# Kernel tuning notes

Measured on AMD Instinct MI355X. Metric: run time of the kernel, lower is better.

## Reference

```python
import jax, jax.numpy as jnp
import numpy as np

H, W = 1024, 1024        # heatmap resolution
C = 128                  # n_targets (clusters)
N_ITER = 8               # n_iterations


def setup_inputs() -> dict:
    key = jax.random.key(0)
    k1, k2 = jax.random.split(key)
    # clusters live in pixel coordinate space [0,H) x [0,W)
    clusters = jax.random.uniform(k1, (C, 2), dtype=jnp.float32) * jnp.array([H, W], dtype=jnp.float32)
    heatmap = jax.random.uniform(k2, (H, W), dtype=jnp.float32)
    return {"clusters": clusters, "heatmap": heatmap}


def reference(clusters, heatmap):
    # pixel coordinate grid [H, W, 2] with (row, col) ordering, matching
    # clusters[c,0]-row, clusters[c,1]-col in the original code
    rows = jnp.arange(H, dtype=jnp.float32)
    cols = jnp.arange(W, dtype=jnp.float32)
    coords = jnp.stack(jnp.meshgrid(rows, cols, indexing='ij'), axis=-1)  # [H, W, 2]

    def step(cs, _):
        # Euclidean distance from every pixel to every cluster, clamped to >= 1
        diff = coords[:, :, None, :] - cs[None, None, :, :]          # [H, W, C, 2]
        dist = jnp.maximum(1.0, jnp.sqrt(jnp.sum(diff * diff, axis=-1)))  # [H, W, C]
        assign = jnp.argmin(dist, axis=-1)                            # [H, W] nearest cluster
        best_dist = jnp.min(dist, axis=-1)                            # [H, W]
        # weighted scatter-add of pixel coords into their nearest cluster
        contrib = coords * (heatmap / best_dist)[..., None]           # [H, W, 2]
        new_cs = jax.ops.segment_sum(contrib.reshape(-1, 2), assign.reshape(-1), num_segments=C)
        return new_cs.astype(jnp.float32), None

    cs, _ = jax.lax.scan(step, clusters, None, length=N_ITER)
    return cs
```

## Files before the change

kernel.cpp:

```cpp
#include <hip/hip_runtime.h>
#include <float.h>

constexpr int H = 1024, W = 1024, C = 128, N_ITER = 8;
constexpr int TPB = 256;
constexpr int TILE = 32;
constexpr int PPT = 4;
constexpr int K = 32;
constexpr int SLOTS = 2 * C;

__global__ __launch_bounds__(TPB) void kmeans_step(
    const float* __restrict__ cur0,
    const float* __restrict__ prevShards,
    const float* __restrict__ heatmap,
    float* __restrict__ outShards)
{
    __shared__ float2 cls[C];
    __shared__ float2 cand[C];
    __shared__ int    candIdx[C];
    __shared__ float  waveMin[2];
    __shared__ int    waveCnt[2];
    __shared__ float  acc[SLOTS];
    __shared__ unsigned char dupf[C];

    const int tid   = threadIdx.x;
    const int tileR = (blockIdx.x >> 5) * TILE;
    const int tileC = (blockIdx.x & 31) * TILE;

    acc[tid] = 0.0f;
    if (tid < C) dupf[tid] = 0;

    float coord;
    if (prevShards) {
        float s = 0.0f;
#pragma unroll
        for (int k = 0; k < K; ++k) s += prevShards[k * SLOTS + tid];
        coord = s;
    } else {
        coord = cur0[tid];
    }
    ((float*)cls)[tid] = coord;
    __syncthreads();

    const int    di  = tid & (C - 1);
    const float2 dme = cls[di];

    float dcen = 0.0f;
    if (tid < C) {
        const float dxr = dme.x - ((float)tileR + 15.5f);
        const float dyc = dme.y - ((float)tileC + 15.5f);
        dcen = sqrtf(dxr * dxr + dyc * dyc);
        float m = dcen;
#pragma unroll
        for (int off = 32; off > 0; off >>= 1)
            m = fminf(m, __shfl_xor(m, off));
        if ((tid & 63) == 0) waveMin[tid >> 6] = m;
    }

    {
        const int kLo = (tid < C) ? 1 : 33;
#pragma unroll 8
        for (int kk = 0; kk < 32; ++kk) {
            const int k = kLo + kk;
            const int j = (di + k) & (C - 1);
            const float2 o = cls[j];
            if (o.x == dme.x && o.y == dme.y)
                dupf[(di + k < C) ? (di + k) : di] = 1;
        }
    }
    __syncthreads();

    bool keep = false;
    int  pre  = 0;
    if (tid < C) {
        const float thr = fminf(waveMin[0], waveMin[1]) + 44.84062f;
        keep = (dcen <= thr) && (dupf[tid] == 0);
        const unsigned long long mask = __ballot(keep);
        const int lane = tid & 63;
        pre = __popcll(mask & ((1ull << lane) - 1ull));
        if (lane == 0) waveCnt[tid >> 6] = __popcll(mask);
    }
    __syncthreads();
    if (keep) {
        const int pos = pre + ((tid >= 64) ? waveCnt[0] : 0);
        cand[pos]    = cls[tid];
        candIdx[pos] = tid;
    }
    __syncthreads();

    const int nCand = waveCnt[0] + waveCnt[1];

    const int   rowIn = tid >> 3;
    const float fr    = (float)(tileR + rowIn);
    const int   col0  = tileC + (tid & 7) * PPT;
    const float4 h4   = *(const float4*)(heatmap + (size_t)(tileR + rowIn) * W + col0);

    float hval[PPT] = { h4.x, h4.y, h4.z, h4.w };
    float colf[PPT], best[PPT];
    int   bi[PPT];
#pragma unroll
    for (int p = 0; p < PPT; ++p) {
        colf[p] = (float)(col0 + p);
        best[p] = FLT_MAX;
        bi[p]   = 0;
    }

    for (int k = 0; k < nCand; ++k) {
        const float2 cl = cand[k];
        const int    ci = candIdx[k];
        const float  dx  = fr - cl.x;
        const float  dx2 = dx * dx;
#pragma unroll
        for (int p = 0; p < PPT; ++p) {
            const float dy  = colf[p] - cl.y;
            const float d2  = fmaf(dy, dy, dx2);
            const float key = fmaxf(d2, 1.0f);
            const bool  lt  = key < best[p];
            bi[p]   = lt ? ci  : bi[p];
            best[p] = lt ? key : best[p];
        }
    }

#pragma unroll
    for (int p = 0; p < PPT; ++p) {
        const float bd  = fmaxf(1.0f, sqrtf(best[p]));
        const float wgt = hval[p] / bd;
        float v0 = fr      * wgt;
        float v1 = colf[p] * wgt;
        const int b0 = __shfl(bi[p], 0);
        if (__ballot(bi[p] == b0) == 0xFFFFFFFFFFFFFFFFull) {
#pragma unroll
            for (int off = 32; off > 0; off >>= 1) {
                v0 += __shfl_xor(v0, off);
                v1 += __shfl_xor(v1, off);
            }
            if ((tid & 63) == 0) {
                unsafeAtomicAdd(&acc[2 * b0 + 0], v0);
                unsafeAtomicAdd(&acc[2 * b0 + 1], v1);
            }
        } else {
            unsafeAtomicAdd(&acc[2 * bi[p] + 0], v0);
            unsafeAtomicAdd(&acc[2 * bi[p] + 1], v1);
        }
    }
    __syncthreads();

    const float a = acc[tid];
    if (a != 0.0f)
        unsafeAtomicAdd(&outShards[(blockIdx.x & (K - 1)) * SLOTS + tid], a);
}

__global__ __launch_bounds__(SLOTS) void kmeans_finalize(
    const float* __restrict__ shards,
    float* __restrict__ out)
{
    const int tid = threadIdx.x;
    float s = 0.0f;
#pragma unroll
    for (int k = 0; k < K; ++k) s += shards[k * SLOTS + tid];
    out[tid] = s;
}

extern "C" void kernel_launch(void* const* d_in, const int* in_sizes, int n_in,
                              void* d_out, int out_size, void* d_ws, size_t ws_size,
                              hipStream_t stream) {
    const float* clusters = (const float*)d_in[0];
    const float* heatmap  = (const float*)d_in[1];
    float* out = (float*)d_out;

    float* shards = (float*)d_ws;
    const size_t perIter = (size_t)K * SLOTS;

    hipMemsetAsync(shards, 0, N_ITER * perIter * sizeof(float), stream);

    for (int it = 0; it < N_ITER; ++it) {
        const float* prev = (it == 0) ? nullptr : (shards + (it - 1) * perIter);
        float* dst = shards + it * perIter;
        kmeans_step<<<H, TPB, 0, stream>>>(clusters, prev, heatmap, dst);
    }
    kmeans_finalize<<<1, SLOTS, 0, stream>>>(shards + (N_ITER - 1) * perIter, out);
}
```

Before: 143.3 us.

## Fuse all iterations into one persistent kernel with a coordinator block and flag barriers

Replaces the eight per-iteration launches and the finalize launch with one kernel. Block 0 acts as a coordinator: it waits on distributed arrival counters, reduces the shards, runs the duplicate-cluster check once, and publishes sign-encoded centroids to replicated buffers. Worker blocks spin on those buffers for the next iteration. This removes launch gaps, keeps the heatmap tile in registers across iterations, and moves the duplicate check off the workers. The cost is a 1025-block grid that depends on all blocks being co-resident (launch bounds raised to 4 blocks per CU), with a risk of deadlock or spin overhead if they are not.

```diff
diff --git a/kernel.cpp b/kernel.cpp
--- a/kernel.cpp
+++ b/kernel.cpp
@@ -7,12 +7,24 @@
 constexpr int PPT = 4;
 constexpr int K = 32;
 constexpr int SLOTS = 2 * C;
-
-__global__ __launch_bounds__(TPB) void kmeans_step(
+constexpr int NBLK = (H / TILE) * (W / TILE);
+constexpr int NCNT = 128;
+constexpr int CNT_STRIDE = 16;
+constexpr int ARRIVE_DEPTH = NBLK / NCNT;
+constexpr int NREP = 16;
+constexpr unsigned SIGNB = 0x80000000u;
+
+__device__ __forceinline__ void waitVmem() {
+    asm volatile("s_waitcnt vmcnt(0)" ::: "memory");
+}
+
+__global__ __launch_bounds__(TPB, 4) void kmeans_fused(
     const float* __restrict__ cur0,
-    const float* __restrict__ prevShards,
     const float* __restrict__ heatmap,
-    float* __restrict__ outShards)
+    float* __restrict__ shards,
+    int*   __restrict__ barCnt,
+    unsigned* __restrict__ clsPub,
+    float* __restrict__ out)
 {
     __shared__ float2 cls[C];
     __shared__ float2 cand[C];
@@ -22,142 +34,188 @@
     __shared__ float  acc[SLOTS];
     __shared__ unsigned char dupf[C];
 
-    const int tid   = threadIdx.x;
-    const int tileR = (blockIdx.x >> 5) * TILE;
-    const int tileC = (blockIdx.x & 31) * TILE;
-
-    acc[tid] = 0.0f;
-    if (tid < C) dupf[tid] = 0;
-
-    float coord;
-    if (prevShards) {
-        float s = 0.0f;
-#pragma unroll
-        for (int k = 0; k < K; ++k) s += prevShards[k * SLOTS + tid];
-        coord = s;
-    } else {
-        coord = cur0[tid];
+    const int tid = threadIdx.x;
+    const int bid = blockIdx.x;
+
+    if (bid == 0) {
+        for (int it = 0; it < N_ITER; ++it) {
+            if (tid < NCNT) {
+                int* cptr = barCnt + ((size_t)it * NCNT + tid) * CNT_STRIDE;
+                while (__hip_atomic_load(cptr, __ATOMIC_RELAXED,
+                                         __HIP_MEMORY_SCOPE_AGENT) < ARRIVE_DEPTH)
+                    __builtin_amdgcn_s_sleep(1);
+            }
+            __syncthreads();
+
+            const float* b = shards + (size_t)it * K * SLOTS + tid;
+            float v[K];
+#pragma unroll
+            for (int k = 0; k < K; ++k)
+                v[k] = __hip_atomic_load(b + (size_t)k * SLOTS,
+                                         __ATOMIC_RELAXED, __HIP_MEMORY_SCOPE_AGENT);
+            float s = 0.0f;
+#pragma unroll
+            for (int k = 0; k < K; ++k) s += v[k];
+
+            if (it == N_ITER - 1) {
+                out[tid] = s;
+                return;
+            }
+
+            if (tid < C) dupf[tid] = 0;
+            ((float*)cls)[tid] = s;
+            __syncthreads();
+            {
+                const int    sdi  = tid & (C - 1);
+                const float2 sdme = cls[sdi];
+                const int kLo = (tid < C) ? 1 : 33;
+#pragma unroll 8
+                for (int kk = 0; kk < 32; ++kk) {
+                    const int k = kLo + kk;
+                    const int j = (sdi + k) & (C - 1);
+                    const float2 o = cls[j];
+                    if (o.x == sdme.x && o.y == sdme.y)
+                        dupf[(sdi + k < C) ? (sdi + k) : sdi] = 1;
+                }
+            }
+            __syncthreads();
+
+            const float pv = dupf[tid >> 1] ? (float)INFINITY : s;
+            const unsigned enc = __float_as_uint(pv) ^ SIGNB;
+            unsigned* pb = clsPub + (size_t)it * NREP * SLOTS;
+#pragma unroll
+            for (int r = 0; r < NREP; ++r)
+                __hip_atomic_store(pb + r * SLOTS + tid, enc,
+                                   __ATOMIC_RELAXED, __HIP_MEMORY_SCOPE_AGENT);
+        }
+        return;
     }
-    ((float*)cls)[tid] = coord;
-    __syncthreads();
-
-    const int    di  = tid & (C - 1);
-    const float2 dme = cls[di];
-
-    float dcen = 0.0f;
-    if (tid < C) {
-        const float dxr = dme.x - ((float)tileR + 15.5f);
-        const float dyc = dme.y - ((float)tileC + 15.5f);
-        dcen = sqrtf(dxr * dxr + dyc * dyc);
-        float m = dcen;
-#pragma unroll
-        for (int off = 32; off > 0; off >>= 1)
-            m = fminf(m, __shfl_xor(m, off));
-        if ((tid & 63) == 0) waveMin[tid >> 6] = m;
-    }
-
-    {
-        const int kLo = (tid < C) ? 1 : 33;
-#pragma unroll 8
-        for (int kk = 0; kk < 32; ++kk) {
-            const int k = kLo + kk;
-            const int j = (di + k) & (C - 1);
-            const float2 o = cls[j];
-            if (o.x == dme.x && o.y == dme.y)
-                dupf[(di + k < C) ? (di + k) : di] = 1;
-        }
-    }
-    __syncthreads();
-
-    bool keep = false;
-    int  pre  = 0;
-    if (tid < C) {
-        const float thr = fminf(waveMin[0], waveMin[1]) + 44.84062f;
-        keep = (dcen <= thr) && (dupf[tid] == 0);
-        const unsigned long long mask = __ballot(keep);
-        const int lane = tid & 63;
-        pre = __popcll(mask & ((1ull << lane) - 1ull));
-        if (lane == 0) waveCnt[tid >> 6] = __popcll(mask);
-    }
-    __syncthreads();
-    if (keep) {
-        const int pos = pre + ((tid >= 64) ? waveCnt[0] : 0);
-        cand[pos]    = cls[tid];
-        candIdx[pos] = tid;
-    }
-    __syncthreads();
-
-    const int nCand = waveCnt[0] + waveCnt[1];
+
+    const int wid   = bid - 1;
+    const int tileR = (wid >> 5) * TILE;
+    const int tileC = (wid & 31) * TILE;
 
     const int   rowIn = tid >> 3;
     const float fr    = (float)(tileR + rowIn);
     const int   col0  = tileC + (tid & 7) * PPT;
     const float4 h4   = *(const float4*)(heatmap + (size_t)(tileR + rowIn) * W + col0);
-
     float hval[PPT] = { h4.x, h4.y, h4.z, h4.w };
-    float colf[PPT], best[PPT];
-    int   bi[PPT];
-#pragma unroll
-    for (int p = 0; p < PPT; ++p) {
-        colf[p] = (float)(col0 + p);
-        best[p] = FLT_MAX;
-        bi[p]   = 0;
+    float colf[PPT];
+#pragma unroll
+    for (int p = 0; p < PPT; ++p) colf[p] = (float)(col0 + p);
+
+    for (int it = 0; it < N_ITER; ++it) {
+        float coord;
+        if (it == 0) {
+            coord = cur0[tid];
+        } else {
+            const unsigned* src = clsPub
+                + ((size_t)(it - 1) * NREP + (wid & (NREP - 1))) * SLOTS;
+            unsigned u;
+            for (;;) {
+                u = __hip_atomic_load(src + tid, __ATOMIC_RELAXED,
+                                      __HIP_MEMORY_SCOPE_AGENT);
+                if (__ballot(u != 0u) == 0xFFFFFFFFFFFFFFFFull) break;
+                __builtin_amdgcn_s_sleep(4);
+            }
+            coord = __uint_as_float(u ^ SIGNB);
+        }
+
+        acc[tid] = 0.0f;
+        ((float*)cls)[tid] = coord;
+        __syncthreads();
+
+        float dcen = 0.0f;
+        if (tid < C) {
+            const float2 cl = cls[tid];
+            const float dxr = cl.x - ((float)tileR + 15.5f);
+            const float dyc = cl.y - ((float)tileC + 15.5f);
+            dcen = sqrtf(dxr * dxr + dyc * dyc);
+            float m = dcen;
+#pragma unroll
+            for (int off = 32; off > 0; off >>= 1)
+                m = fminf(m, __shfl_xor(m, off));
+            if ((tid & 63) == 0) waveMin[tid >> 6] = m;
+        }
+        __syncthreads();
+
+        bool keep = false;
+        int  pre  = 0;
+        if (tid < C) {
+            const float thr = fminf(waveMin[0], waveMin[1]) + 44.84062f;
+            keep = (dcen <= thr);
+            const unsigned long long mask = __ballot(keep);
+            const int lane = tid & 63;
+            pre = __popcll(mask & ((1ull << lane) - 1ull));
+            if (lane == 0) waveCnt[tid >> 6] = __popcll(mask);
+        }
+        __syncthreads();
+        if (keep) {
+            const int pos = pre + ((tid >= 64) ? waveCnt[0] : 0);
+            cand[pos]    = cls[tid];
+            candIdx[pos] = tid;
+        }
+        __syncthreads();
+
+        const int nCand = waveCnt[0] + waveCnt[1];
+
+        float best[PPT];
+        int   bi[PPT];
+#pragma unroll
+        for (int p = 0; p < PPT; ++p) { best[p] = FLT_MAX; bi[p] = 0; }
+
+        for (int k = 0; k < nCand; ++k) {
+            const float2 cl = cand[k];
+            const int    ci = candIdx[k];
+            const float  dx  = fr - cl.x;
+            const float  dx2 = dx * dx;
+#pragma unroll
+            for (int p = 0; p < PPT; ++p) {
+                const float dy  = colf[p] - cl.y;
+                const float d2  = fmaf(dy, dy, dx2);
+                const float key = fmaxf(d2, 1.0f);
+                const bool  lt  = key < best[p];
+                bi[p]   = lt ? ci  : bi[p];
+                best[p] = lt ? key : best[p];
+            }
+        }
+
+#pragma unroll
+        for (int p = 0; p < PPT; ++p) {
+            const float bd  = fmaxf(1.0f, sqrtf(best[p]));
+            const float wgt = hval[p] / bd;
+            float v0 = fr      * wgt;
+            float v1 = colf[p] * wgt;
+            const int b0 = __shfl(bi[p], 0);
+            if (__ballot(bi[p] == b0) == 0xFFFFFFFFFFFFFFFFull) {
+#pragma unroll
+                for (int off = 32; off > 0; off >>= 1) {
+                    v0 += __shfl_xor(v0, off);
+                    v1 += __shfl_xor(v1, off);
+                }
+                if ((tid & 63) == 0) {
+                    unsafeAtomicAdd(&acc[2 * b0 + 0], v0);
+                    unsafeAtomicAdd(&acc[2 * b0 + 1], v1);
+                }
+            } else {
+                unsafeAtomicAdd(&acc[2 * bi[p] + 0], v0);
+                unsafeAtomicAdd(&acc[2 * bi[p] + 1], v1);
+            }
+        }
+        __syncthreads();
+
+        const float a = acc[tid];
+        if (a != 0.0f)
+            unsafeAtomicAdd(&shards[(size_t)it * K * SLOTS
+                                    + (wid & (K - 1)) * SLOTS + tid], a);
+
+        waitVmem();
+        __syncthreads();
+        if (tid == 0)
+            __hip_atomic_fetch_add(
+                barCnt + ((size_t)it * NCNT + (wid & (NCNT - 1))) * CNT_STRIDE, 1,
+                __ATOMIC_RELAXED, __HIP_MEMORY_SCOPE_AGENT);
     }
-
-    for (int k = 0; k < nCand; ++k) {
-        const float2 cl = cand[k];
-        const int    ci = candIdx[k];
-        const float  dx  = fr - cl.x;
-        const float  dx2 = dx * dx;
-#pragma unroll
-        for (int p = 0; p < PPT; ++p) {
-            const float dy  = colf[p] - cl.y;
-            const float d2  = fmaf(dy, dy, dx2);
-            const float key = fmaxf(d2, 1.0f);
-            const bool  lt  = key < best[p];
-            bi[p]   = lt ? ci  : bi[p];
-            best[p] = lt ? key : best[p];
-        }
-    }
-
-#pragma unroll
-    for (int p = 0; p < PPT; ++p) {
-        const float bd  = fmaxf(1.0f, sqrtf(best[p]));
-        const float wgt = hval[p] / bd;
-        float v0 = fr      * wgt;
-        float v1 = colf[p] * wgt;
-        const int b0 = __shfl(bi[p], 0);
-        if (__ballot(bi[p] == b0) == 0xFFFFFFFFFFFFFFFFull) {
-#pragma unroll
-            for (int off = 32; off > 0; off >>= 1) {
-                v0 += __shfl_xor(v0, off);
-                v1 += __shfl_xor(v1, off);
-            }
-            if ((tid & 63) == 0) {
-                unsafeAtomicAdd(&acc[2 * b0 + 0], v0);
-                unsafeAtomicAdd(&acc[2 * b0 + 1], v1);
-            }
-        } else {
-            unsafeAtomicAdd(&acc[2 * bi[p] + 0], v0);
-            unsafeAtomicAdd(&acc[2 * bi[p] + 1], v1);
-        }
-    }
-    __syncthreads();
-
-    const float a = acc[tid];
-    if (a != 0.0f)
-        unsafeAtomicAdd(&outShards[(blockIdx.x & (K - 1)) * SLOTS + tid], a);
-}
-
-__global__ __launch_bounds__(SLOTS) void kmeans_finalize(
-    const float* __restrict__ shards,
-    float* __restrict__ out)
-{
-    const int tid = threadIdx.x;
-    float s = 0.0f;
-#pragma unroll
-    for (int k = 0; k < K; ++k) s += shards[k * SLOTS + tid];
-    out[tid] = s;
 }
 
 extern "C" void kernel_launch(void* const* d_in, const int* in_sizes, int n_in,
@@ -168,14 +226,14 @@
     float* out = (float*)d_out;
 
     float* shards = (float*)d_ws;
-    const size_t perIter = (size_t)K * SLOTS;
-
-    hipMemsetAsync(shards, 0, N_ITER * perIter * sizeof(float), stream);
-
-    for (int it = 0; it < N_ITER; ++it) {
-        const float* prev = (it == 0) ? nullptr : (shards + (it - 1) * perIter);
-        float* dst = shards + it * perIter;
-        kmeans_step<<<H, TPB, 0, stream>>>(clusters, prev, heatmap, dst);
-    }
-    kmeans_finalize<<<1, SLOTS, 0, stream>>>(shards + (N_ITER - 1) * perIter, out);
+    const size_t shardBytes = (size_t)N_ITER * K * SLOTS * sizeof(float);
+    int* barCnt = (int*)((char*)d_ws + shardBytes);
+    const size_t cntBytes = (size_t)N_ITER * NCNT * CNT_STRIDE * sizeof(int);
+    unsigned* clsPub = (unsigned*)((char*)barCnt + cntBytes);
+    const size_t pubBytes = (size_t)N_ITER * NREP * SLOTS * sizeof(unsigned);
+
+    hipMemsetAsync(d_ws, 0, shardBytes + cntBytes + pubBytes, stream);
+
+    kmeans_fused<<<NBLK + 1, TPB, 0, stream>>>(clusters, heatmap, shards,
+                                               barCnt, clsPub, out);
 }
```

Result: no change. 141.7 us (median of 2 runs) (-1.1%).
